# Optimization experiments

Measured on AMD Instinct MI355X. Metric: run time of the kernel, lower is better.

## Reference

```python
import jax, jax.numpy as jnp
import numpy as np

NUM_HEADS = 12

def _pe(L, d):
    # standard sinusoidal positional encoding, shape (1, L, d)
    pos = jnp.arange(L, dtype=jnp.float32)[:, None]
    i = jnp.arange(d)[None, :]
    angle = pos / jnp.power(10000.0, (2 * (i // 2)).astype(jnp.float32) / d)
    pe = jnp.where(i % 2 == 0, jnp.sin(angle), jnp.cos(angle))
    return pe[None]

def _ln(x, scale, bias, eps=1e-5):
    m = x.mean(-1, keepdims=True)
    v = ((x - m) ** 2).mean(-1, keepdims=True)
    return (x - m) / jnp.sqrt(v + eps) * scale + bias

def setup_inputs() -> dict:
    key = jax.random.key(0)
    ks = jax.random.split(key, 8)
    D = 768
    s = 0.02
    return {
        "x": jax.random.normal(ks[0], (8, D, 32, 32), jnp.float32),
        "context_token": jax.random.normal(ks[1], (1, 1, D), jnp.float32),
        "register_tokens": jax.random.normal(ks[2], (1, 4, D), jnp.float32),
        "in_proj_w": jax.random.normal(ks[3], (3 * D, D), jnp.float32) * s,
        "in_proj_b": jnp.zeros((3 * D,), jnp.float32),
        "out_proj_w": jax.random.normal(ks[4], (D, D), jnp.float32) * s,
        "out_proj_b": jnp.zeros((D,), jnp.float32),
        "ln1_s": jnp.ones((D,), jnp.float32),
        "ln1_b": jnp.zeros((D,), jnp.float32),
        "ln2_s": jnp.ones((D,), jnp.float32),
        "ln2_b": jnp.zeros((D,), jnp.float32),
        "ffn_w1": jax.random.normal(ks[5], (4 * D, D), jnp.float32) * s,
        "ffn_b1": jnp.zeros((4 * D,), jnp.float32),
        "ffn_w2": jax.random.normal(ks[6], (D, 4 * D), jnp.float32) * s,
        "ffn_b2": jnp.zeros((D,), jnp.float32),
    }

def reference(x, context_token, register_tokens, in_proj_w, in_proj_b,
              out_proj_w, out_proj_b, ln1_s, ln1_b, ln2_s, ln2_b,
              ffn_w1, ffn_b1, ffn_w2, ffn_b2):
    B, d, h, w = x.shape
    N = h * w
    R = register_tokens.shape[1]
    G = 1 + R  # global tokens: context + registers
    nh = NUM_HEADS
    dh = d // nh
    # (B, N, d)
    x_flat = x.reshape(B, d, N).transpose(0, 2, 1)
    tokens = jnp.concatenate([
        jnp.broadcast_to(context_token, (B, 1, d)),
        jnp.broadcast_to(register_tokens, (B, R, d)),
    ], axis=1)
    tokens = tokens + _pe(G, d)
    xwt = _ln(jnp.concatenate([tokens, x_flat], axis=1), ln1_s, ln1_b)
    S = G + N
    # MultiheadAttention (eval mode, dropout off): fused in-projection
    qkv = xwt @ in_proj_w.T + in_proj_b
    q, k, v = jnp.split(qkv, 3, axis=-1)
    to_heads = lambda t: t.reshape(B, S, nh, dh).transpose(0, 2, 1, 3)
    q, k, v = to_heads(q), to_heads(k), to_heads(v)
    scores = jnp.einsum('bhqd,bhkd->bhqk', q, k) / np.float32(np.sqrt(dh))
    # mask (True = disallowed): feature rows (>=G) cannot attend to global cols (<G);
    # global rows attend everything; feature-feature block allowed.
    row_feat = jnp.arange(S) >= G
    col_glob = jnp.arange(S) < G
    disallowed = row_feat[:, None] & col_glob[None, :]
    scores = jnp.where(disallowed, -jnp.inf, scores)
    attn = jax.nn.softmax(scores, axis=-1)
    o = jnp.einsum('bhqk,bhkd->bhqd', attn, v).transpose(0, 2, 1, 3).reshape(B, S, d)
    o = o @ out_proj_w.T + out_proj_b
    y = o + xwt
    ff = jax.nn.gelu(_ln(y, ln2_s, ln2_b) @ ffn_w1.T + ffn_b1, approximate=False) @ ffn_w2.T + ffn_b2
    y = y + ff
    context_out = y[:, 0:1, :]
    register_out = y[:, 1:G, :]
    feature_out = y[:, G:, :].transpose(0, 2, 1).reshape(B, d, h, w)
    return feature_out, context_out, register_out
```

## Files before the change

kernel.cpp:

```cpp
#include <hip/hip_runtime.h>
#include <hip/hip_bf16.h>
#include <cmath>

typedef unsigned short u16;
typedef __bf16 bf16x8 __attribute__((ext_vector_type(8)));
typedef float floatx4 __attribute__((ext_vector_type(4)));

#define SQ 1029
#define DM 768
#define NH 12
#define SQP 1088
#define SSC 0.18033688011112042f

#define GLD16(gp, lp) __builtin_amdgcn_global_load_lds( \
    (const __attribute__((address_space(1))) unsigned int*)(gp), \
    (__attribute__((address_space(3))) unsigned int*)(lp), 16, 0, 0)

#define OFF_WQKV ((size_t)0)
#define OFF_WOUT ((size_t)3538944)
#define OFF_W1   ((size_t)4718592)
#define OFF_W2   ((size_t)9437184)
#define OFF_XF   ((size_t)14155776)
#define OFF_XWT  ((size_t)26800128)
#define OFF_QKV  ((size_t)39444480)
#define OFF_VT   ((size_t)77783040)
#define OFF_Y    ((size_t)91152384)
#define OFF_BQ   ((size_t)103796736)

__device__ __forceinline__ float bf2f(u16 u) {
  unsigned int x = ((unsigned int)u) << 16;
  float f; __builtin_memcpy(&f, &x, 4); return f;
}
__device__ __forceinline__ u16 f2bf(float f) {
  unsigned int x; __builtin_memcpy(&x, &f, 4);
  x = (x + 0x7fffu + ((x >> 16) & 1u)) >> 16;
  return (u16)x;
}
__device__ __forceinline__ unsigned int pk_bf16(float a, float b) {
  __hip_bfloat162 h = __float22bfloat162_rn(make_float2(a, b));
  unsigned int u; __builtin_memcpy(&u, &h, 4); return u;
}

__device__ __forceinline__ void blockReduce2(float& s1, float& s2) {
  #pragma unroll
  for (int o = 32; o > 0; o >>= 1) { s1 += __shfl_xor(s1, o); s2 += __shfl_xor(s2, o); }
  __shared__ float t1[4], t2[4];
  const int w = threadIdx.x >> 6;
  if ((threadIdx.x & 63) == 0) { t1[w] = s1; t2[w] = s2; }
  __syncthreads();
  s1 = t1[0] + t1[1] + t1[2] + t1[3];
  s2 = t2[0] + t2[1] + t2[2] + t2[3];
}

__global__ __launch_bounds__(256) void convw_all(
    const float* __restrict__ a, const float* __restrict__ b,
    const float* __restrict__ c, const float* __restrict__ d, u16* __restrict__ dst) {
  int i = blockIdx.x * 256 + threadIdx.x;
  if (i >= 1769472) return;
  const float* src; int off;
  if (i < 442368)       { src = a; off = i; }
  else if (i < 589824)  { src = b; off = i - 442368; }
  else if (i < 1179648) { src = c; off = i - 589824; }
  else                  { src = d; off = i - 1179648; }
  float4 v = ((const float4*)src)[off];
  if (i < 147456) { v.x *= SSC; v.y *= SSC; v.z *= SSC; v.w *= SSC; }
  ushort4 o; o.x = f2bf(v.x); o.y = f2bf(v.y); o.z = f2bf(v.z); o.w = f2bf(v.w);
  ((ushort4*)dst)[i] = o;
}

__global__ __launch_bounds__(256) void convb(const float* __restrict__ b, float* __restrict__ o) {
  int i = blockIdx.x * 256 + threadIdx.x;
  if (i >= 2304) return;
  o[i] = (i < 768) ? b[i] * SSC : b[i];
}

__global__ __launch_bounds__(256) void transpose_x(const float* __restrict__ x, u16* __restrict__ xf) {
  __shared__ u16 tile[32][33];
  const int b = blockIdx.x, ct = blockIdx.y, nt = blockIdx.z;
  const int i = threadIdx.x, jj = threadIdx.y;
  #pragma unroll
  for (int kk = 0; kk < 4; ++kk) {
    int j = jj + kk * 8;
    tile[j][i] = f2bf(x[((size_t)b * 768 + ct * 32 + j) * 1024 + nt * 32 + i]);
  }
  __syncthreads();
  #pragma unroll
  for (int kk = 0; kk < 4; ++kk) {
    int j = jj + kk * 8;
    xf[((size_t)b * 1024 + nt * 32 + j) * 768 + ct * 32 + i] = tile[i][j];
  }
}

__global__ __launch_bounds__(256) void build_xwt(
    const u16* __restrict__ xf, const float* __restrict__ ctx, const float* __restrict__ regt,
    const float* __restrict__ g, const float* __restrict__ be, u16* __restrict__ xwt) {
  const int row = blockIdx.x;
  const int b = row / SQ, s = row % SQ;
  const int tid = threadIdx.x;
  float v[3];
  #pragma unroll
  for (int i = 0; i < 3; ++i) {
    const int c = tid + i * 256;
    float val;
    if (s >= 5) {
      val = bf2f(xf[((size_t)b * 1024 + (s - 5)) * DM + c]);
    } else {
      float tok = (s == 0) ? ctx[c] : regt[(s - 1) * DM + c];
      float e = (float)(2 * (c / 2)) * (1.0f / 768.0f);
      float ang = (float)s / powf(10000.0f, e);
      val = tok + ((c & 1) ? cosf(ang) : sinf(ang));
    }
    v[i] = val;
  }
  float s1 = v[0] + v[1] + v[2];
  float s2 = v[0] * v[0] + v[1] * v[1] + v[2] * v[2];
  blockReduce2(s1, s2);
  const float mean = s1 * (1.0f / 768.0f);
  const float var = s2 * (1.0f / 768.0f) - mean * mean;
  const float rs = rsqrtf(fmaxf(var, 0.0f) + 1e-5f);
  #pragma unroll
  for (int i = 0; i < 3; ++i) {
    const int c = tid + i * 256;
    xwt[(size_t)row * DM + c] = f2bf((v[i] - mean) * rs * g[c] + be[c]);
  }
}

__global__ __launch_bounds__(256) void ln2k(
    const u16* __restrict__ y, const float* __restrict__ g, const float* __restrict__ be,
    u16* __restrict__ out) {
  const int row = blockIdx.x;
  const int tid = threadIdx.x;
  float v[3];
  #pragma unroll
  for (int i = 0; i < 3; ++i) v[i] = bf2f(y[(size_t)row * DM + tid + i * 256]);
  float s1 = v[0] + v[1] + v[2];
  float s2 = v[0] * v[0] + v[1] * v[1] + v[2] * v[2];
  blockReduce2(s1, s2);
  const float mean = s1 * (1.0f / 768.0f);
  const float var = s2 * (1.0f / 768.0f) - mean * mean;
  const float rs = rsqrtf(fmaxf(var, 0.0f) + 1e-5f);
  #pragma unroll
  for (int i = 0; i < 3; ++i) {
    const int c = tid + i * 256;
    out[(size_t)row * DM + c] = f2bf((v[i] - mean) * rs * g[c] + be[c]);
  }
}

template<int EPI, int K, int NB>
__global__ __launch_bounds__(512, 2) void gemm256(
    const u16* __restrict__ A, const u16* __restrict__ W, const float* __restrict__ bias,
    const u16* __restrict__ res, u16* __restrict__ out, int M) {
  constexpr int N = NB * 256;
  constexpr int NT = K / 64;
  extern __shared__ __align__(16) char SMb[];
  const int tid = threadIdx.x, wave = tid >> 6, lane = tid & 63, quad = lane >> 4, l16 = lane & 15;
  const int wm = wave >> 2, wn = wave & 3;
  const int lin = blockIdx.x;
  int mb, nb;
  if (lin < 32 * NB) { const int g = lin / (8 * NB); const int r = lin - g * 8 * NB; mb = g * 8 + (r & 7); nb = r >> 3; }
  else { mb = 32; nb = lin - 32 * NB; }
  const int m0 = mb * 256, n0 = nb * 256;

  const u16* Ap[4]; const u16* Wp[4];
  #pragma unroll
  for (int it = 0; it < 4; ++it) {
    const int c = it * 512 + tid;
    const int row = c >> 3, gch = (c & 7) ^ (row & 7);
    Ap[it] = A + (size_t)min(m0 + row, M - 1) * K + gch * 8;
    Wp[it] = W + (size_t)(n0 + row) * K + gch * 8;
  }
  char* asl = SMb + tid * 16;
  char* bsl = SMb + 65536 + tid * 16;

  auto STAGE = [&](int ts, int slot) {
    const int ko = ts * 64;
    #pragma unroll
    for (int it = 0; it < 4; ++it) GLD16(Ap[it] + ko, asl + slot * 32768 + it * 8192);
    #pragma unroll
    for (int it = 0; it < 4; ++it) GLD16(Wp[it] + ko, bsl + slot * 32768 + it * 8192);
  };

  floatx4 acc[8][4];
  #pragma unroll
  for (int i = 0; i < 8; ++i)
    #pragma unroll
    for (int j = 0; j < 4; ++j) { floatx4 z = {0.f, 0.f, 0.f, 0.f}; acc[i][j] = z; }

  const int ch0 = (quad ^ (l16 & 7)) << 3;
  const int ch1 = ((4 + quad) ^ (l16 & 7)) << 3;

  STAGE(0, 0); STAGE(1, 1);

  #pragma unroll 1
  for (int t = 0; t < NT; ++t) {
    if (t < NT - 1) { asm volatile("s_waitcnt vmcnt(8)" ::: "memory"); }
    else            { asm volatile("s_waitcnt vmcnt(0)" ::: "memory"); }
    __builtin_amdgcn_s_barrier();
    __builtin_amdgcn_sched_barrier(0);
    const u16* As = (const u16*)(SMb + (t & 1) * 32768);
    const u16* Bs = (const u16*)(SMb + 65536 + (t & 1) * 32768);
    bf16x8 a0[8], b0[4], a1[8], b1[4];
    #pragma unroll
    for (int i = 0; i < 8; ++i) a0[i] = *(const bf16x8*)&As[(wm * 128 + i * 16 + l16) * 64 + ch0];
    #pragma unroll
    for (int j = 0; j < 4; ++j) b0[j] = *(const bf16x8*)&Bs[(wn * 64 + j * 16 + l16) * 64 + ch0];
    __builtin_amdgcn_s_setprio(1);
    #pragma unroll
    for (int i = 0; i < 8; ++i)
      #pragma unroll
      for (int j = 0; j < 4; ++j)
        acc[i][j] = __builtin_amdgcn_mfma_f32_16x16x32_bf16(b0[j], a0[i], acc[i][j], 0, 0, 0);
    __builtin_amdgcn_s_setprio(0);
    #pragma unroll
    for (int i = 0; i < 8; ++i) a1[i] = *(const bf16x8*)&As[(wm * 128 + i * 16 + l16) * 64 + ch1];
    #pragma unroll
    for (int j = 0; j < 4; ++j) b1[j] = *(const bf16x8*)&Bs[(wn * 64 + j * 16 + l16) * 64 + ch1];
    asm volatile("s_waitcnt lgkmcnt(0)" ::: "memory");
    __builtin_amdgcn_sched_barrier(0);
    __builtin_amdgcn_s_barrier();
    __builtin_amdgcn_sched_barrier(0);
    if (t + 2 < NT) STAGE(t + 2, t & 1);
    __builtin_amdgcn_sched_barrier(0);
    __builtin_amdgcn_s_setprio(1);
    #pragma unroll
    for (int i = 0; i < 8; ++i)
      #pragma unroll
      for (int j = 0; j < 4; ++j)
        acc[i][j] = __builtin_amdgcn_mfma_f32_16x16x32_bf16(b1[j], a1[i], acc[i][j], 0, 0, 0);
    __builtin_amdgcn_s_setprio(0);
  }

  #pragma unroll
  for (int j = 0; j < 4; ++j) {
    const float4 b4 = *(const float4*)(bias + n0 + wn * 64 + j * 16 + quad * 4);
    #pragma unroll
    for (int i = 0; i < 8; ++i) {
      acc[i][j][0] += b4.x; acc[i][j][1] += b4.y; acc[i][j][2] += b4.z; acc[i][j][3] += b4.w;
    }
  }
  if constexpr (EPI == 2) {
    #pragma unroll
    for (int i = 0; i < 8; ++i)
      #pragma unroll
      for (int j = 0; j < 4; ++j)
        #pragma unroll
        for (int r = 0; r < 4; ++r) {
          const float v = acc[i][j][r];
          acc[i][j][r] = v / (1.0f + exp2f(-2.3022221f * (v + 0.044715f * v * v * v)));
        }
  }
  u16* Ep = (u16*)SMb + wave * 2304;
  #pragma unroll
  for (int g = 0; g < 4; ++g) {
    #pragma unroll
    for (int i2 = 0; i2 < 2; ++i2) {
      const int i = g * 2 + i2;
      #pragma unroll
      for (int j = 0; j < 4; ++j) {
        uint2 w;
        w.x = pk_bf16(acc[i][j][0], acc[i][j][1]);
        w.y = pk_bf16(acc[i][j][2], acc[i][j][3]);
        *(uint2*)&Ep[(i2 * 16 + l16) * 72 + j * 16 + quad * 4] = w;
      }
    }
    #pragma unroll
    for (int s = 0; s < 4; ++s) {
      const int lrow = s * 8 + (lane >> 3);
      const int gm = m0 + wm * 128 + g * 32 + lrow;
      const int gn = n0 + wn * 64 + (lane & 7) * 8;
      uint4 lv = *(const uint4*)&Ep[lrow * 72 + (lane & 7) * 8];
      if constexpr (EPI == 1 || EPI == 3) {
        const uint4 rv = *(const uint4*)(res + (size_t)min(gm, M - 1) * N + gn);
        const unsigned* lp = &lv.x; const unsigned* rp = &rv.x;
        uint4 ov; unsigned* op = &ov.x;
        #pragma unroll
        for (int d = 0; d < 4; ++d) {
          const float a0 = bf2f((u16)(lp[d] & 0xffffu)) + bf2f((u16)(rp[d] & 0xffffu));
          const float a1 = bf2f((u16)(lp[d] >> 16)) + bf2f((u16)(rp[d] >> 16));
          op[d] = pk_bf16(a0, a1);
        }
        lv = ov;
      }
      if (gm < M) *(uint4*)(out + (size_t)gm * N + gn) = lv;
    }
  }
}

__global__ __launch_bounds__(256) void vtrans(const u16* __restrict__ qkv, u16* __restrict__ vt) {
  __shared__ u16 t[32][33];
  const int bh = blockIdx.x, st = blockIdx.y, dt = blockIdx.z;
  const int bq = bh / NH, hh = bh % NH;
  u16* vd = vt + (size_t)bh * 64 * SQP;
  const int i = threadIdx.x, jj = threadIdx.y;
  #pragma unroll
  for (int kk = 0; kk < 4; ++kk) {
    int j = jj + kk * 8;
    t[j][i] = qkv[(size_t)(bq * SQ + st * 32 + j) * 2304 + 1536 + hh * 64 + dt * 32 + i];
  }
  __syncthreads();
  #pragma unroll
  for (int kk = 0; kk < 4; ++kk) {
    int j = jj + kk * 8;
    vd[(size_t)(dt * 32 + j) * SQP + st * 32 + i] = t[i][j];
  }
}

__global__ __launch_bounds__(256) void attn_flash(
    const u16* __restrict__ qkv, const u16* __restrict__ vt, u16* __restrict__ out) {
  const int bh = blockIdx.x, qt = blockIdx.y;
  const int b = bh / NH, h = bh % NH;
  const int tid = threadIdx.x, wave = tid >> 6, lane = tid & 63, quad = lane >> 4, l16 = lane & 15;
  __shared__ u16 Qs[4096], Ks[4096], VTs[4096];
  __shared__ u16 Ps[64 * 72];
  const int q0 = qt * 64;
  const u16* qk = qkv + (size_t)b * SQ * 2304 + h * 64;
  const u16* vslab = vt + (size_t)bh * 64 * SQP;
  const int c0 = tid, c1 = tid + 256;
  const int r0 = c0 >> 3, q0c = (c0 & 7) ^ (r0 & 7);
  const int r1 = c1 >> 3, q1c = (c1 & 7) ^ (r1 & 7);
  u16* L0Q = Qs + wave * 512;  u16* L1Q = Qs + 2048 + wave * 512;
  u16* L0K = Ks + wave * 512;  u16* L1K = Ks + 2048 + wave * 512;
  u16* L0V = VTs + wave * 512; u16* L1V = VTs + 2048 + wave * 512;

  GLD16(qk + (size_t)(q0 + r0) * 2304 + q0c * 8, L0Q);
  GLD16(qk + (size_t)(q0 + r1) * 2304 + q1c * 8, L1Q);

  floatx4 Oa[4];
  #pragma unroll
  for (int nt = 0; nt < 4; ++nt) { floatx4 z = {0.f, 0.f, 0.f, 0.f}; Oa[nt] = z; }
  float l_acc = 0.f;
  const int qrow = wave * 16 + l16;
  const bool qfeat = (q0 + qrow >= 5);
  bf16x8 qf0, qf1;

  for (int t = 0; t < 17; ++t) {
    const int k0 = t * 64;
    __syncthreads();
    GLD16(qk + 768 + (size_t)(k0 + r0) * 2304 + q0c * 8, L0K);
    GLD16(qk + 768 + (size_t)(k0 + r1) * 2304 + q1c * 8, L1K);
    GLD16(vslab + (size_t)r0 * SQP + k0 + q0c * 8, L0V);
    GLD16(vslab + (size_t)r1 * SQP + k0 + q1c * 8, L1V);
    __syncthreads();

    if (t == 0) {
      qf0 = *(const bf16x8*)&Qs[qrow * 64 + ((quad ^ (qrow & 7)) << 3)];
      qf1 = *(const bf16x8*)&Qs[qrow * 64 + (((4 + quad) ^ (qrow & 7)) << 3)];
    }

    floatx4 st[4];
    #pragma unroll
    for (int mt = 0; mt < 4; ++mt) { floatx4 z = {0.f, 0.f, 0.f, 0.f}; st[mt] = z; }
    #pragma unroll
    for (int kk = 0; kk < 2; ++kk) {
      const bf16x8 qf = kk ? qf1 : qf0;
      #pragma unroll
      for (int mt = 0; mt < 4; ++mt) {
        const int krow = mt * 16 + l16;
        bf16x8 kf = *(const bf16x8*)&Ks[krow * 64 + (((kk * 4 + quad) ^ (krow & 7)) << 3)];
        st[mt] = __builtin_amdgcn_mfma_f32_16x16x32_bf16(kf, qf, st[mt], 0, 0, 0);
      }
    }

    if (t == 16) {
      float p[4];
      #pragma unroll
      for (int r = 0; r < 4; ++r) {
        float pv = exp2f(st[0][r]);
        p[r] = (quad * 4 + r < 5) ? pv : 0.f;
      }
      l_acc += (p[0] + p[1]) + (p[2] + p[3]);
      uint2 w;
      w.x = pk_bf16(p[0], p[1]);
      w.y = pk_bf16(p[2], p[3]);
      *(uint2*)&Ps[qrow * 72 + quad * 4] = w;
      const uint2 zz = {0u, 0u};
      #pragma unroll
      for (int mt = 1; mt < 4; ++mt) *(uint2*)&Ps[qrow * 72 + mt * 16 + quad * 4] = zz;
    } else if (t == 0) {
      #pragma unroll
      for (int mt = 0; mt < 4; ++mt) {
        float p[4];
        #pragma unroll
        for (int r = 0; r < 4; ++r) {
          float pv = exp2f(st[mt][r]);
          if (mt == 0) pv = (qfeat && (quad * 4 + r < 5)) ? 0.f : pv;
          p[r] = pv;
        }
        l_acc += (p[0] + p[1]) + (p[2] + p[3]);
        uint2 w;
        w.x = pk_bf16(p[0], p[1]);
        w.y = pk_bf16(p[2], p[3]);
        *(uint2*)&Ps[qrow * 72 + mt * 16 + quad * 4] = w;
      }
    } else {
      #pragma unroll
      for (int mt = 0; mt < 4; ++mt) {
        float p[4];
        #pragma unroll
        for (int r = 0; r < 4; ++r) p[r] = exp2f(st[mt][r]);
        l_acc += (p[0] + p[1]) + (p[2] + p[3]);
        uint2 w;
        w.x = pk_bf16(p[0], p[1]);
        w.y = pk_bf16(p[2], p[3]);
        *(uint2*)&Ps[qrow * 72 + mt * 16 + quad * 4] = w;
      }
    }

    auto pv_step = [&](int kk) {
      bf16x8 pf = *(const bf16x8*)&Ps[qrow * 72 + kk * 32 + quad * 8];
      #pragma unroll
      for (int nt = 0; nt < 4; ++nt) {
        const int brow = nt * 16 + l16;
        bf16x8 bb = *(const bf16x8*)&VTs[brow * 64 + (((kk * 4 + quad) ^ (brow & 7)) << 3)];
        Oa[nt] = __builtin_amdgcn_mfma_f32_16x16x32_bf16(pf, bb, Oa[nt], 0, 0, 0);
      }
    };
    pv_step(0);
    if (t != 16) pv_step(1);
  }

  float lt = l_acc;
  lt += __shfl_xor(lt, 16);
  lt += __shfl_xor(lt, 32);
  lt = fmaxf(lt, 1e-30f);
  #pragma unroll
  for (int nt = 0; nt < 4; ++nt)
    #pragma unroll
    for (int r = 0; r < 4; ++r) {
      const int qo = quad * 4 + r;
      const float lr = __shfl(lt, (lane & 48) | qo);
      const int qg2 = q0 + wave * 16 + qo;
      if (qg2 < SQ)
        out[((size_t)b * SQ + qg2) * DM + h * 64 + nt * 16 + l16] = f2bf(Oa[nt][r] / lr);
    }
}

__global__ __launch_bounds__(256) void transpose_out(const u16* __restrict__ yf, float* __restrict__ out) {
  __shared__ u16 tile[32][33];
  const int b = blockIdx.x, nt = blockIdx.y, ct = blockIdx.z;
  const int i = threadIdx.x, jj = threadIdx.y;
  #pragma unroll
  for (int kk = 0; kk < 4; ++kk) {
    int j = jj + kk * 8;
    tile[j][i] = yf[((size_t)b * SQ + 5 + nt * 32 + j) * DM + ct * 32 + i];
  }
  __syncthreads();
  #pragma unroll
  for (int kk = 0; kk < 4; ++kk) {
    int j = jj + kk * 8;
    out[((size_t)b * 768 + ct * 32 + j) * 1024 + nt * 32 + i] = bf2f(tile[i][j]);
  }
}

__global__ __launch_bounds__(256) void out_small(const u16* __restrict__ yf, float* __restrict__ out) {
  const int idx = blockIdx.x * 256 + threadIdx.x;
  if (idx >= 8 * 5 * DM) return;
  const int b = idx / (5 * DM);
  const int r = idx % (5 * DM);
  const int s = r / DM, c = r % DM;
  const float v = bf2f(yf[((size_t)b * SQ + s) * DM + c]);
  if (s == 0) out[(size_t)6291456 + (size_t)b * DM + c] = v;
  else out[(size_t)6291456 + 6144 + ((size_t)b * 4 + (s - 1)) * DM + c] = v;
}

extern "C" void kernel_launch(void* const* d_in, const int* in_sizes, int n_in,
                              void* d_out, int out_size, void* d_ws, size_t ws_size,
                              hipStream_t stream) {
  const float* x    = (const float*)d_in[0];
  const float* ctx  = (const float*)d_in[1];
  const float* regt = (const float*)d_in[2];
  const float* wqkv = (const float*)d_in[3];
  const float* bqkv = (const float*)d_in[4];
  const float* wout = (const float*)d_in[5];
  const float* bout = (const float*)d_in[6];
  const float* ln1s = (const float*)d_in[7];
  const float* ln1b = (const float*)d_in[8];
  const float* ln2s = (const float*)d_in[9];
  const float* ln2b = (const float*)d_in[10];
  const float* w1   = (const float*)d_in[11];
  const float* b1   = (const float*)d_in[12];
  const float* w2   = (const float*)d_in[13];
  const float* b2   = (const float*)d_in[14];

  char* ws = (char*)d_ws;
  u16* wb_all = (u16*)(ws + OFF_WQKV);
  u16* wqkv_b = (u16*)(ws + OFF_WQKV);
  u16* wout_b = (u16*)(ws + OFF_WOUT);
  u16* w1_b   = (u16*)(ws + OFF_W1);
  u16* w2_b   = (u16*)(ws + OFF_W2);
  u16* xf     = (u16*)(ws + OFF_XF);
  u16* xwt    = (u16*)(ws + OFF_XWT);
  u16* qkv    = (u16*)(ws + OFF_QKV);
  u16* vtb    = (u16*)(ws + OFF_VT);
  u16* yb     = (u16*)(ws + OFF_Y);
  float* bqs  = (float*)(ws + OFF_BQ);
  u16* attnb  = (u16*)(ws + OFF_XF);
  u16* ynorm  = (u16*)(ws + OFF_XF);
  u16* h1     = (u16*)(ws + OFF_QKV);
  u16* yfin   = (u16*)(ws + OFF_XWT);
  float* outp = (float*)d_out;

  static bool attr_done = false;
  if (!attr_done) {
    attr_done = true;
    hipFuncSetAttribute(reinterpret_cast<const void*>(&gemm256<0, 768, 9>),
                        hipFuncAttributeMaxDynamicSharedMemorySize, 131072);
    hipFuncSetAttribute(reinterpret_cast<const void*>(&gemm256<1, 768, 3>),
                        hipFuncAttributeMaxDynamicSharedMemorySize, 131072);
    hipFuncSetAttribute(reinterpret_cast<const void*>(&gemm256<2, 768, 12>),
                        hipFuncAttributeMaxDynamicSharedMemorySize, 131072);
    hipFuncSetAttribute(reinterpret_cast<const void*>(&gemm256<3, 3072, 3>),
                        hipFuncAttributeMaxDynamicSharedMemorySize, 131072);
  }

  convw_all   <<<6912, 256, 0, stream>>>(wqkv, wout, w1, w2, wb_all);
  convb       <<<9, 256, 0, stream>>>(bqkv, bqs);
  transpose_x <<<dim3(8, 24, 32), dim3(32, 8), 0, stream>>>(x, xf);
  build_xwt   <<<8232, 256, 0, stream>>>(xf, ctx, regt, ln1s, ln1b, xwt);
  gemm256<0, 768, 9><<<33 * 9, 512, 131072, stream>>>(xwt, wqkv_b, bqs, nullptr, qkv, 8232);
  vtrans      <<<dim3(96, 34, 2), dim3(32, 8), 0, stream>>>(qkv, vtb);
  attn_flash  <<<dim3(96, 17), 256, 0, stream>>>(qkv, vtb, attnb);
  gemm256<1, 768, 3><<<33 * 3, 512, 131072, stream>>>(attnb, wout_b, bout, xwt, yb, 8232);
  ln2k        <<<8232, 256, 0, stream>>>(yb, ln2s, ln2b, ynorm);
  gemm256<2, 768, 12><<<33 * 12, 512, 131072, stream>>>(ynorm, w1_b, b1, nullptr, h1, 8232);
  gemm256<3, 3072, 3><<<33 * 3, 512, 131072, stream>>>(h1, w2_b, b2, yb, yfin, 8232);
  transpose_out<<<dim3(8, 32, 24), dim3(32, 8), 0, stream>>>(yfin, outp);
  out_small   <<<120, 256, 0, stream>>>(yfin, outp);
}
```

Before: 439.3 us.

## Restructure 256x256 GEMM main loop into four interleaved quadrant phases

The GEMM K-loop is reorganized so each wave computes its 8x4 accumulator tile in four quadrant phases. Each phase loads only the LDS fragments it needs, and the global-to-LDS loads for upcoming K slices are split into half-tile pieces issued between phases. The goal is to overlap global memory traffic with MFMA work more finely and to cut register pressure from holding whole fragment sets, so the 2-blocks-per-CU occupancy holds with less stall at barriers. The cost is more barriers per iteration and more intricate vmcnt bookkeeping. Redundant clamped loads in the tail iterations add a little wasted traffic.

```diff
diff --git a/kernel.cpp b/kernel.cpp
--- a/kernel.cpp
+++ b/kernel.cpp
@@ -161,24 +161,26 @@
   else { mb = 32; nb = lin - 32 * NB; }
   const int m0 = mb * 256, n0 = nb * 256;
 
-  const u16* Ap[4]; const u16* Wp[4];
-  #pragma unroll
-  for (int it = 0; it < 4; ++it) {
-    const int c = it * 512 + tid;
-    const int row = c >> 3, gch = (c & 7) ^ (row & 7);
-    Ap[it] = A + (size_t)min(m0 + row, M - 1) * K + gch * 8;
-    Wp[it] = W + (size_t)(n0 + row) * K + gch * 8;
-  }
-  char* asl = SMb + tid * 16;
-  char* bsl = SMb + 65536 + tid * 16;
-
-  auto STAGE = [&](int ts, int slot) {
-    const int ko = ts * 64;
-    #pragma unroll
-    for (int it = 0; it < 4; ++it) GLD16(Ap[it] + ko, asl + slot * 32768 + it * 8192);
-    #pragma unroll
-    for (int it = 0; it < 4; ++it) GLD16(Wp[it] + ko, bsl + slot * 32768 + it * 8192);
+  const int c0r = tid >> 3, c0g = ((tid & 7) ^ (c0r & 7)) * 8;
+  const u16* Aq[2][2]; const u16* Wq[2][2];
+  #pragma unroll
+  for (int h = 0; h < 2; ++h) {
+    #pragma unroll
+    for (int it = 0; it < 2; ++it) {
+      const int row = h * 128 + it * 64 + c0r;
+      Aq[it][h] = A + (size_t)min(m0 + row, M - 1) * K + c0g;
+      Wq[it][h] = W + (size_t)(n0 + row) * K + c0g;
+    }
+  }
+
+  auto SA = [&](int kc, int h, int sl) {
+    GLD16(Aq[0][h] + kc * 64, SMb + sl * 32768 + h * 16384 + tid * 16);
+    GLD16(Aq[1][h] + kc * 64, SMb + sl * 32768 + h * 16384 + 8192 + tid * 16);
   };
+  auto SB = [&](int kc, int h, int sl) {
+    GLD16(Wq[0][h] + kc * 64, SMb + 65536 + sl * 32768 + h * 16384 + tid * 16);
+    GLD16(Wq[1][h] + kc * 64, SMb + 65536 + sl * 32768 + h * 16384 + 8192 + tid * 16);
+  };
 
   floatx4 acc[8][4];
   #pragma unroll
@@ -186,49 +188,108 @@
     #pragma unroll
     for (int j = 0; j < 4; ++j) { floatx4 z = {0.f, 0.f, 0.f, 0.f}; acc[i][j] = z; }
 
-  const int ch0 = (quad ^ (l16 & 7)) << 3;
-  const int ch1 = ((4 + quad) ^ (l16 & 7)) << 3;
-
-  STAGE(0, 0); STAGE(1, 1);
+  const int chk0 = (quad ^ (l16 & 7)) << 3;
+  const int chk1 = ((4 + quad) ^ (l16 & 7)) << 3;
+
+  SA(0, 0, 0); SA(0, 1, 0); SB(0, 0, 0); SB(0, 1, 0);
+  SB(1, 0, 1); SB(1, 1, 1); SA(1, 0, 1);
+  asm volatile("s_waitcnt vmcnt(6)" ::: "memory");
+  __builtin_amdgcn_sched_barrier(0);
+  __builtin_amdgcn_s_barrier();
+
+  bf16x8 a0[8], a1[8], b0[4], b1[4];
 
   #pragma unroll 1
   for (int t = 0; t < NT; ++t) {
-    if (t < NT - 1) { asm volatile("s_waitcnt vmcnt(8)" ::: "memory"); }
-    else            { asm volatile("s_waitcnt vmcnt(0)" ::: "memory"); }
+    const int sl = t & 1, nx = sl ^ 1;
+    const u16* Sa = (const u16*)SMb + sl * 16384 + wm * 8192;
+    const u16* Sb = (const u16*)SMb + 32768 + sl * 16384 + (wn >> 1) * 8192;
+    const int brow = (wn & 1) * 64;
+    const int kA = min(t + 1, NT - 1), kB = min(t + 2, NT - 1);
+
+    #pragma unroll
+    for (int i = 0; i < 4; ++i) {
+      a0[i] = *(const bf16x8*)&Sa[(i * 16 + l16) * 64 + chk0];
+      a1[i] = *(const bf16x8*)&Sa[(i * 16 + l16) * 64 + chk1];
+    }
+    #pragma unroll
+    for (int j = 0; j < 2; ++j) {
+      b0[j] = *(const bf16x8*)&Sb[(brow + j * 16 + l16) * 64 + chk0];
+      b1[j] = *(const bf16x8*)&Sb[(brow + j * 16 + l16) * 64 + chk1];
+    }
+    asm volatile("s_waitcnt lgkmcnt(0)" ::: "memory");
+    __builtin_amdgcn_sched_barrier(0);
+    __builtin_amdgcn_s_setprio(1);
+    #pragma unroll
+    for (int i = 0; i < 4; ++i)
+      #pragma unroll
+      for (int j = 0; j < 2; ++j) {
+        acc[i][j] = __builtin_amdgcn_mfma_f32_16x16x32_bf16(b0[j], a0[i], acc[i][j], 0, 0, 0);
+        acc[i][j] = __builtin_amdgcn_mfma_f32_16x16x32_bf16(b1[j], a1[i], acc[i][j], 0, 0, 0);
+      }
+    __builtin_amdgcn_s_setprio(0);
+    __builtin_amdgcn_sched_barrier(0);
     __builtin_amdgcn_s_barrier();
-    __builtin_amdgcn_sched_barrier(0);
-    const u16* As = (const u16*)(SMb + (t & 1) * 32768);
-    const u16* Bs = (const u16*)(SMb + 65536 + (t & 1) * 32768);
-    bf16x8 a0[8], b0[4], a1[8], b1[4];
-    #pragma unroll
-    for (int i = 0; i < 8; ++i) a0[i] = *(const bf16x8*)&As[(wm * 128 + i * 16 + l16) * 64 + ch0];
-    #pragma unroll
-    for (int j = 0; j < 4; ++j) b0[j] = *(const bf16x8*)&Bs[(wn * 64 + j * 16 + l16) * 64 + ch0];
+
+    #pragma unroll
+    for (int j = 2; j < 4; ++j) {
+      b0[j] = *(const bf16x8*)&Sb[(brow + j * 16 + l16) * 64 + chk0];
+      b1[j] = *(const bf16x8*)&Sb[(brow + j * 16 + l16) * 64 + chk1];
+    }
+    SA(kA, 1, nx);
+    asm volatile("s_waitcnt lgkmcnt(0)" ::: "memory");
+    __builtin_amdgcn_sched_barrier(0);
     __builtin_amdgcn_s_setprio(1);
     #pragma unroll
-    for (int i = 0; i < 8; ++i)
-      #pragma unroll
-      for (int j = 0; j < 4; ++j)
+    for (int i = 0; i < 4; ++i)
+      #pragma unroll
+      for (int j = 2; j < 4; ++j) {
         acc[i][j] = __builtin_amdgcn_mfma_f32_16x16x32_bf16(b0[j], a0[i], acc[i][j], 0, 0, 0);
+        acc[i][j] = __builtin_amdgcn_mfma_f32_16x16x32_bf16(b1[j], a1[i], acc[i][j], 0, 0, 0);
+      }
     __builtin_amdgcn_s_setprio(0);
-    #pragma unroll
-    for (int i = 0; i < 8; ++i) a1[i] = *(const bf16x8*)&As[(wm * 128 + i * 16 + l16) * 64 + ch1];
-    #pragma unroll
-    for (int j = 0; j < 4; ++j) b1[j] = *(const bf16x8*)&Bs[(wn * 64 + j * 16 + l16) * 64 + ch1];
+    __builtin_amdgcn_sched_barrier(0);
+    __builtin_amdgcn_s_barrier();
+
+    #pragma unroll
+    for (int i = 4; i < 8; ++i) {
+      a0[i] = *(const bf16x8*)&Sa[(i * 16 + l16) * 64 + chk0];
+      a1[i] = *(const bf16x8*)&Sa[(i * 16 + l16) * 64 + chk1];
+    }
+    SB(kB, 0, sl);
     asm volatile("s_waitcnt lgkmcnt(0)" ::: "memory");
     __builtin_amdgcn_sched_barrier(0);
+    __builtin_amdgcn_s_setprio(1);
+    #pragma unroll
+    for (int i = 4; i < 8; ++i)
+      #pragma unroll
+      for (int j = 2; j < 4; ++j) {
+        acc[i][j] = __builtin_amdgcn_mfma_f32_16x16x32_bf16(b0[j], a0[i], acc[i][j], 0, 0, 0);
+        acc[i][j] = __builtin_amdgcn_mfma_f32_16x16x32_bf16(b1[j], a1[i], acc[i][j], 0, 0, 0);
+      }
+    __builtin_amdgcn_s_setprio(0);
+    __builtin_amdgcn_sched_barrier(0);
     __builtin_amdgcn_s_barrier();
-    __builtin_amdgcn_sched_barrier(0);
-    if (t + 2 < NT) STAGE(t + 2, t & 1);
+
+    SB(kB, 1, sl);
+    SA(kB, 0, sl);
     __builtin_amdgcn_sched_barrier(0);
     __builtin_amdgcn_s_setprio(1);
     #pragma unroll
-    for (int i = 0; i < 8; ++i)
-      #pragma unroll
-      for (int j = 0; j < 4; ++j)
+    for (int i = 4; i < 8; ++i)
+      #pragma unroll
+      for (int j = 0; j < 2; ++j) {
+        acc[i][j] = __builtin_amdgcn_mfma_f32_16x16x32_bf16(b0[j], a0[i], acc[i][j], 0, 0, 0);
         acc[i][j] = __builtin_amdgcn_mfma_f32_16x16x32_bf16(b1[j], a1[i], acc[i][j], 0, 0, 0);
+      }
     __builtin_amdgcn_s_setprio(0);
-  }
+    asm volatile("s_waitcnt vmcnt(6)" ::: "memory");
+    __builtin_amdgcn_sched_barrier(0);
+    __builtin_amdgcn_s_barrier();
+  }
+
+  asm volatile("s_waitcnt vmcnt(0)" ::: "memory");
+  __builtin_amdgcn_s_barrier();
 
   #pragma unroll
   for (int j = 0; j < 4; ++j) {
@@ -275,9 +336,9 @@
         uint4 ov; unsigned* op = &ov.x;
         #pragma unroll
         for (int d = 0; d < 4; ++d) {
-          const float a0 = bf2f((u16)(lp[d] & 0xffffu)) + bf2f((u16)(rp[d] & 0xffffu));
-          const float a1 = bf2f((u16)(lp[d] >> 16)) + bf2f((u16)(rp[d] >> 16));
-          op[d] = pk_bf16(a0, a1);
+          const float p0 = bf2f((u16)(lp[d] & 0xffffu)) + bf2f((u16)(rp[d] & 0xffffu));
+          const float p1 = bf2f((u16)(lp[d] >> 16)) + bf2f((u16)(rp[d] >> 16));
+          op[d] = pk_bf16(p0, p1);
         }
         lv = ov;
       }
```

Result: no change. 435.3 us (-0.9%).
